# Kernel optimization log

Hardware: AMD Instinct MI355X
Metric: run time of the kernel (lower is better)

## Reference

```python
import jax, jax.numpy as jnp
import numpy as np

N, E, H, MID = 4096, 384, 6, 96  # n_refs, embed_dim, num_heads, mlp mid dim (max(E//4,32))
DH = E // H  # head dim = 64


def setup_inputs() -> dict:
    key = jax.random.key(0)
    ks = jax.random.split(key, 12)
    def w(k, shape, fan_in):
        return jax.random.normal(k, shape, jnp.float32) / np.float32(np.sqrt(fan_in))
    return {
        "low": jax.random.normal(ks[0], (N, E), jnp.float32),
        "high": jax.random.normal(ks[1], (N, E), jnp.float32),
        "ref_w": jax.random.uniform(ks[2], (N,), jnp.float32) + 0.1,
        "low_w1": w(ks[3], (E, MID), E), "low_b1": jnp.zeros((MID,), jnp.float32),
        "low_w2": w(ks[4], (MID, E), MID), "low_b2": jnp.zeros((E,), jnp.float32),
        "high_w1": w(ks[5], (E, MID), E), "high_b1": jnp.zeros((MID,), jnp.float32),
        "high_w2": w(ks[6], (MID, E), MID), "high_b2": jnp.zeros((E,), jnp.float32),
        "layer_fuse": jnp.array([0.4, 0.6], jnp.float32),
        "wqkv": w(ks[7], (E, 3 * E), E), "bqkv": jnp.zeros((3 * E,), jnp.float32),
        "wo": w(ks[8], (E, E), E), "bo": jnp.zeros((E,), jnp.float32),
        "ln_g": jnp.ones((E,), jnp.float32), "ln_b": jnp.zeros((E,), jnp.float32),
    }


def _channel_mlp(x, w1, b1, w2, b2):
    h = jax.nn.gelu(x @ w1 + b1, approximate=False)  # [N, MID]
    return x * jax.nn.sigmoid(h @ w2 + b2)           # [N, E]


def _forward(low, high, ref_w, low_w1, low_b1, low_w2, low_b2,
             high_w1, high_b1, high_w2, high_b2, layer_fuse,
             wqkv, bqkv, wo, bo, ln_g, ln_b):
    lw = jax.nn.softmax(layer_fuse)
    fused = lw[0] * _channel_mlp(low, low_w1, low_b1, low_w2, low_b2) \
          + lw[1] * _channel_mlp(high, high_w1, high_b1, high_w2, high_b2)  # [N, E]
    # single-layer MHA over the n-reference sequence (batch of 1, batch_first)
    qkv = fused @ wqkv + bqkv                      # [N, 3E]
    q, k, v = jnp.split(qkv, 3, axis=-1)
    q = q.reshape(N, H, DH).transpose(1, 0, 2)     # [H, N, DH]
    k = k.reshape(N, H, DH).transpose(1, 0, 2)
    v = v.reshape(N, H, DH).transpose(1, 0, 2)
    scores = jnp.einsum("hnd,hmd->hnm", q, k) / np.float32(np.sqrt(DH))
    attn = jax.nn.softmax(scores, axis=-1)         # [H, N, N]
    ctx = jnp.einsum("hnm,hmd->hnd", attn, v)      # [H, N, DH]
    attn_out = ctx.transpose(1, 0, 2).reshape(N, E) @ wo + bo
    x = attn_out + fused                           # residual
    mu = jnp.mean(x, axis=-1, keepdims=True)
    var = jnp.mean(jnp.square(x - mu), axis=-1, keepdims=True)
    x = (x - mu) / jnp.sqrt(var + 1e-5) * ln_g + ln_b
    w = ref_w / jnp.sum(ref_w)
    res = jnp.sum(x * w[:, None], axis=0)          # weighted mean over refs -> [E]
    return res / (jnp.linalg.norm(res) + 1e-8)


def reference(low, high, ref_w, low_w1, low_b1, low_w2, low_b2,
              high_w1, high_b1, high_w2, high_b2, layer_fuse,
              wqkv, bqkv, wo, bo, ln_g, ln_b):
    return _forward(low, high, ref_w, low_w1, low_b1, low_w2, low_b2,
                    high_w1, high_b1, high_w2, high_b2, layer_fuse,
                    wqkv, bqkv, wo, bo, ln_g, ln_b)
```

## Files before the change

kernel.cpp:

```cpp
#include <hip/hip_runtime.h>
#include <math.h>

#define Nn 4096
#define Ee 384
#define Hh 6
#define DHh 64
#define MIDm 96
#define TEe 1152
#define SPLIT 8

typedef short s16x8 __attribute__((ext_vector_type(8)));
typedef float f32x4 __attribute__((ext_vector_type(4)));
typedef float f32x16 __attribute__((ext_vector_type(16)));
typedef unsigned short ushort_t;
typedef unsigned short ushort4_t __attribute__((ext_vector_type(4)));

#define CROW(r, hf) ((((r) & 3)) + 8 * ((r) >> 2) + 4 * (hf))

__device__ __forceinline__ float gelu_exact(float x) {
    return 0.5f * x * (1.0f + erff(x * 0.70710678118654752f));
}
__device__ __forceinline__ float sigmoidf_(float x) {
    return 1.0f / (1.0f + __expf(-x));
}
__device__ __forceinline__ ushort_t f2bf(float x) {
    unsigned int u = __float_as_uint(x);
    u = (u + 0x7FFFu + ((u >> 16) & 1u)) >> 16;
    return (ushort_t)u;
}
__device__ __forceinline__ float bf2f(ushort_t u) {
    return __uint_as_float(((unsigned int)u) << 16);
}
__device__ __forceinline__ unsigned int cvtpk(float a, float b) {
    unsigned int r;
    asm("v_cvt_pk_bf16_f32 %0, %1, %2" : "=v"(r) : "v"(a), "v"(b));
    return r;
}
__device__ __forceinline__ void gld16(const ushort_t* g, ushort_t* l) {
    __builtin_amdgcn_global_load_lds(
        (const __attribute__((address_space(1))) unsigned int*)g,
        (__attribute__((address_space(3))) unsigned int*)l, 16, 0, 0);
}

#define W1L_OFF 0
#define W1H_OFF 36864
#define W2L_OFF 73728
#define W2H_OFF 110592
#define WQKV_OFF 147456
#define WO_OFF 589824

__global__ __launch_bounds__(256) void k_cvt(
    const float* __restrict__ lw1, const float* __restrict__ hw1,
    const float* __restrict__ lw2, const float* __restrict__ hw2,
    const float* __restrict__ wqkv, const float* __restrict__ wo,
    ushort_t* __restrict__ wT) {
    __shared__ float tl[32][33];
    const int b = blockIdx.x;
    const float* src;
    int R, C, doff, ti;
    if (b < 36)       { src = lw1;  R = 384; C = 96;   doff = W1L_OFF;  ti = b; }
    else if (b < 72)  { src = hw1;  R = 384; C = 96;   doff = W1H_OFF;  ti = b - 36; }
    else if (b < 108) { src = lw2;  R = 96;  C = 384;  doff = W2L_OFF;  ti = b - 72; }
    else if (b < 144) { src = hw2;  R = 96;  C = 384;  doff = W2H_OFF;  ti = b - 108; }
    else if (b < 576) { src = wqkv; R = 384; C = 1152; doff = WQKV_OFF; ti = b - 144; }
    else              { src = wo;   R = 384; C = 384;  doff = WO_OFF;   ti = b - 576; }
    const int tcn = C >> 5;
    const int tr = ti / tcn, tc = ti % tcn;
    const int col = threadIdx.x & 31, r8 = threadIdx.x >> 5;
#pragma unroll
    for (int i = 0; i < 4; i++) {
        const int row = r8 + 8 * i;
        tl[row][col] = src[(size_t)(tr * 32 + row) * C + tc * 32 + col];
    }
    __syncthreads();
#pragma unroll
    for (int i = 0; i < 4; i++) {
        const int rowp = r8 + 8 * i;
        wT[doff + (size_t)(tc * 32 + rowp) * R + tr * 32 + col] = f2bf(tl[col][rowp]);
    }
}

__global__ __launch_bounds__(256) void k_mlp(
    const float* __restrict__ low, const float* __restrict__ high,
    const float* __restrict__ lf, const ushort_t* __restrict__ wT,
    const float* __restrict__ lb1, const float* __restrict__ lb2,
    const float* __restrict__ hb1, const float* __restrict__ hb2,
    ushort_t* __restrict__ fusedb) {
    __shared__ float redsg[6144];
    __shared__ ushort_t Hs[2][16][104];
    float* red = redsg;
    ushort_t* Sg = (ushort_t*)redsg;
    const int t = threadIdx.x;
    const int w = t >> 6, l = t & 63, l15 = l & 15, g4 = l >> 4;
    const int st = w >> 1, kh = w & 1;
    const int rb = blockIdx.x * 16;
    const float* Xf = st ? high : low;
    const ushort_t* w1T = wT + (st ? W1H_OFF : W1L_OFF);
    const ushort_t* w2T = wT + (st ? W2H_OFF : W2L_OFF);
    {
        f32x4 hA[6];
#pragma unroll
        for (int nt = 0; nt < 6; nt++) hA[nt] = (f32x4){0.f, 0.f, 0.f, 0.f};
        for (int ks = 0; ks < 6; ks++) {
            const float* ap = &Xf[(size_t)(rb + l15) * 384 + kh * 192 + ks * 32 + g4 * 8];
            f32x4 a0 = *(const f32x4*)ap;
            f32x4 a1 = *(const f32x4*)(ap + 4);
            union { unsigned int uw[4]; s16x8 v; } ua;
            ua.uw[0] = cvtpk(a0[0], a0[1]);
            ua.uw[1] = cvtpk(a0[2], a0[3]);
            ua.uw[2] = cvtpk(a1[0], a1[1]);
            ua.uw[3] = cvtpk(a1[2], a1[3]);
#pragma unroll
            for (int nt = 0; nt < 6; nt++) {
                s16x8 bf = *(const s16x8*)&w1T[(nt * 16 + l15) * 384 + kh * 192 + ks * 32 + g4 * 8];
                hA[nt] = __builtin_amdgcn_mfma_f32_16x16x32_bf16(ua.v, bf, hA[nt], 0, 0, 0);
            }
        }
#pragma unroll
        for (int nt = 0; nt < 6; nt++)
#pragma unroll
            for (int r = 0; r < 4; r++)
                red[((st * 2 + kh) * 16 + g4 * 4 + r) * 96 + nt * 16 + l15] = hA[nt][r];
    }
    __syncthreads();
    for (int idx = t; idx < 2 * 16 * 96; idx += 256) {
        const int st2 = idx / 1536, rem = idx % 1536;
        const int rowm = rem / 96, mc = rem % 96;
        const float v = red[((st2 * 2) * 16 + rowm) * 96 + mc] +
                        red[((st2 * 2 + 1) * 16 + rowm) * 96 + mc] +
                        (st2 ? hb1[mc] : lb1[mc]);
        Hs[st2][rowm][mc] = f2bf(gelu_exact(v));
    }
    __syncthreads();
    {
        const float* b2p = st ? hb2 : lb2;
        f32x4 sA[12];
#pragma unroll
        for (int nt = 0; nt < 12; nt++) sA[nt] = (f32x4){0.f, 0.f, 0.f, 0.f};
#pragma unroll
        for (int ks = 0; ks < 3; ks++) {
            s16x8 af = *(const s16x8*)&Hs[st][l15][ks * 32 + g4 * 8];
#pragma unroll
            for (int nt = 0; nt < 12; nt++) {
                s16x8 bf = *(const s16x8*)&w2T[(kh * 192 + nt * 16 + l15) * 96 + ks * 32 + g4 * 8];
                sA[nt] = __builtin_amdgcn_mfma_f32_16x16x32_bf16(af, bf, sA[nt], 0, 0, 0);
            }
        }
#pragma unroll
        for (int nt = 0; nt < 12; nt++) {
            const float bb = b2p[kh * 192 + nt * 16 + l15];
#pragma unroll
            for (int r = 0; r < 4; r++)
                Sg[(st * 16 + g4 * 4 + r) * 384 + kh * 192 + nt * 16 + l15] =
                    f2bf(sigmoidf_(sA[nt][r] + bb));
        }
    }
    __syncthreads();
    {
        const float a0 = lf[0], a1 = lf[1];
        const float mx = fmaxf(a0, a1);
        const float e0 = __expf(a0 - mx), e1 = __expf(a1 - mx);
        const float inv = 1.0f / (e0 + e1);
        const float w0 = e0 * inv, w1v = e1 * inv;
        for (int base = t * 4; base < 16 * 384; base += 256 * 4) {
            const int row = base / 384, e0i = base % 384;
            const int gr = rb + row;
            f32x4 lo4 = *(const f32x4*)&low[(size_t)gr * 384 + e0i];
            f32x4 hi4 = *(const f32x4*)&high[(size_t)gr * 384 + e0i];
            ushort4_t s0 = *(const ushort4_t*)&Sg[row * 384 + e0i];
            ushort4_t s1 = *(const ushort4_t*)&Sg[(16 + row) * 384 + e0i];
            ushort4_t fb;
#pragma unroll
            for (int i = 0; i < 4; i++)
                fb[i] = f2bf(w0 * lo4[i] * bf2f(s0[i]) + w1v * hi4[i] * bf2f(s1[i]));
            *(ushort4_t*)&fusedb[(size_t)gr * 384 + e0i] = fb;
        }
    }
}

__global__ __launch_bounds__(256) void k_qkv(
    const ushort_t* __restrict__ fusedb, const ushort_t* __restrict__ wT,
    const float* __restrict__ bqkv,
    ushort_t* __restrict__ qb, ushort_t* __restrict__ kb, ushort_t* __restrict__ vtb) {
    __shared__ float tls[4][32][40];
    const int t = threadIdx.x;
    const int w = t >> 6, l = t & 63, ll = l & 31, hf = l >> 5;
    const int mh = w >> 1, nh = w & 1;
    const int rb = blockIdx.x * 64 + mh * 32;
    const int cb = blockIdx.y * 192 + nh * 96;
    const ushort_t* wq = wT + WQKV_OFF;
    f32x16 acc[3];
#pragma unroll
    for (int nt = 0; nt < 3; nt++)
#pragma unroll
        for (int r = 0; r < 16; r++) acc[nt][r] = 0.0f;
    for (int ks = 0; ks < 24; ks++) {
        s16x8 af = *(const s16x8*)&fusedb[(size_t)(rb + ll) * 384 + ks * 16 + hf * 8];
#pragma unroll
        for (int nt = 0; nt < 3; nt++) {
            s16x8 bf = *(const s16x8*)&wq[(size_t)(cb + nt * 32 + ll) * 384 + ks * 16 + hf * 8];
            acc[nt] = __builtin_amdgcn_mfma_f32_32x32x16_bf16(af, bf, acc[nt], 0, 0, 0);
        }
    }
#pragma unroll
    for (int nt = 0; nt < 3; nt++) {
        const int nb = cb + nt * 32;
        const int which = nb / 384, wn = nb % 384;
        const int hb = wn >> 6, d0 = wn & 63;
        const float bias = bqkv[nb + ll];
        if (which == 2) {
            const int d = d0 + ll;
#pragma unroll
            for (int g2 = 0; g2 < 4; g2++) {
                ushort4_t u4;
#pragma unroll
                for (int i2 = 0; i2 < 4; i2++) u4[i2] = f2bf(acc[nt][g2 * 4 + i2] + bias);
                *(ushort4_t*)&vtb[((size_t)(hb * 64 + d)) * Nn + rb + 8 * g2 + 4 * hf] = u4;
            }
        } else {
            const float sc = (which == 0) ? 0.18033688f : 1.0f;
#pragma unroll
            for (int r = 0; r < 16; r++) tls[w][CROW(r, hf)][ll] = (acc[nt][r] + bias) * sc;
            ushort_t* dst = which ? kb : qb;
            const int row2 = l >> 1, sg = l & 1;
            union { ushort_t us[16]; s16x8 v[2]; } u;
#pragma unroll
            for (int j = 0; j < 16; j++) u.us[j] = f2bf(tls[w][row2][sg * 16 + j]);
            size_t base = ((size_t)hb * Nn + rb + row2) * 64 + d0 + sg * 16;
            *(s16x8*)&dst[base] = u.v[0];
            *(s16x8*)&dst[base + 8] = u.v[1];
        }
    }
}

__global__ __launch_bounds__(512) void k_attn(
    const ushort_t* __restrict__ qb, const ushort_t* __restrict__ kb,
    const ushort_t* __restrict__ vtb, ushort_t* __restrict__ pof,
    float* __restrict__ pml) {
    __shared__ ushort_t Kt[2][4096];
    __shared__ ushort_t Vt[2][4096];
    const int t = threadIdx.x;
    const int wid8 = t >> 6, l = t & 63, ll = l & 31, hf = l >> 5;
    const int lid = blockIdx.x;
    const int xcd = lid & 7, gi = lid >> 3;
    const int pair = xcd * 6 + (gi >> 4);
    const int qt = gi & 15;
    const int h = pair % Hh, sp = pair / Hh;
    const int qrow0 = qt * 256 + wid8 * 32;
    const int srow = t >> 3;
    const int sslot = ((l & 7) ^ (l >> 3)) * 8;
    const int wch = wid8 * 512;
    const ushort_t* kbase = kb + (size_t)h * Nn * DHh;
    const ushort_t* vbase = vtb + (size_t)h * DHh * Nn;
    const int kst0 = sp * (Nn / SPLIT);
#define NT (Nn / (64 * SPLIT))
#define STAGE(B, TI) { const int ktb2 = kst0 + (TI) * 64;                                \
        gld16(kbase + (size_t)(ktb2 + srow) * DHh + sslot, &Kt[B][wch]);                 \
        gld16(vbase + (size_t)srow * Nn + ktb2 + sslot, &Vt[B][wch]); }

    s16x8 qf[4];
#pragma unroll
    for (int dc = 0; dc < 4; dc++)
        qf[dc] = *(const s16x8*)&qb[((size_t)h * Nn + qrow0 + ll) * DHh + dc * 16 + hf * 8];
    f32x16 o0, o1;
#pragma unroll
    for (int r = 0; r < 16; r++) { o0[r] = 0.0f; o1[r] = 0.0f; }
    float lsum = 0.0f;
    const int xorl = (ll & 7) << 3;

    STAGE(0, 0);
    __syncthreads();
    for (int kt = 0; kt < NT; kt++) {
        const int cur = kt & 1;
        if (kt < NT - 1) STAGE(cur ^ 1, kt + 1);
        const ushort_t* KtC = Kt[cur];
        const ushort_t* VtC = Vt[cur];
        f32x16 s0, s1;
#pragma unroll
        for (int r = 0; r < 16; r++) { s0[r] = 0.0f; s1[r] = 0.0f; }
        __builtin_amdgcn_s_setprio(1);
#pragma unroll
        for (int dc = 0; dc < 4; dc++) {
            const int colE = dc * 16 + hf * 8;
            s16x8 kf0 = *(const s16x8*)&KtC[ll * 64 + (colE ^ xorl)];
            s16x8 kf1 = *(const s16x8*)&KtC[(32 + ll) * 64 + (colE ^ xorl)];
            s0 = __builtin_amdgcn_mfma_f32_32x32x16_bf16(kf0, qf[dc], s0, 0, 0, 0);
            s1 = __builtin_amdgcn_mfma_f32_32x32x16_bf16(kf1, qf[dc], s1, 0, 0, 0);
        }
        __builtin_amdgcn_s_setprio(0);
#pragma unroll
        for (int r = 0; r < 16; r++) { s0[r] = exp2f(s0[r]); lsum += s0[r]; }
#pragma unroll
        for (int r = 0; r < 16; r++) { s1[r] = exp2f(s1[r]); lsum += s1[r]; }
#pragma unroll
        for (int ks = 0; ks < 4; ks++) {
            const f32x16 S = (ks < 2) ? s0 : s1;
            const int b = (ks & 1) * 8;
            unsigned int t1 = cvtpk(S[b + 0], S[b + 1]);
            unsigned int t3 = cvtpk(S[b + 2], S[b + 3]);
            unsigned int t2 = cvtpk(S[b + 4], S[b + 5]);
            unsigned int t4 = cvtpk(S[b + 6], S[b + 7]);
            asm("v_permlane32_swap_b32 %0, %1" : "+v"(t1), "+v"(t2));
            asm("v_permlane32_swap_b32 %0, %1" : "+v"(t3), "+v"(t4));
            union { unsigned int uw[4]; s16x8 v; } u;
            u.uw[0] = t1;
            u.uw[1] = t3;
            u.uw[2] = t2;
            u.uw[3] = t4;
            const int colE = ks * 16 + hf * 8;
            s16x8 vf0 = *(const s16x8*)&VtC[ll * 64 + (colE ^ xorl)];
            s16x8 vf1 = *(const s16x8*)&VtC[(32 + ll) * 64 + (colE ^ xorl)];
            o0 = __builtin_amdgcn_mfma_f32_32x32x16_bf16(vf0, u.v, o0, 0, 0, 0);
            o1 = __builtin_amdgcn_mfma_f32_32x32x16_bf16(vf1, u.v, o1, 0, 0, 0);
        }
        __syncthreads();
    }
    lsum += __shfl_xor(lsum, 32, 64);
#pragma unroll
    for (int r = 0; r < 16; r++) {
        const int d_a = CROW(r, hf), d_b = 32 + CROW(r, hf);
        pof[((size_t)(sp * Ee + h * 64 + d_a)) * Nn + qrow0 + ll] = f2bf(o0[r]);
        pof[((size_t)(sp * Ee + h * 64 + d_b)) * Nn + qrow0 + ll] = f2bf(o1[r]);
    }
    if (hf == 0)
        pml[((size_t)sp * Hh + h) * Nn + qrow0 + ll] = lsum;
#undef STAGE
#undef NT
}

__global__ __launch_bounds__(256) void k_oln(
    const ushort_t* __restrict__ pof, const float* __restrict__ pml,
    const ushort_t* __restrict__ wT, const float* __restrict__ bo,
    const ushort_t* __restrict__ fusedb,
    const float* __restrict__ lng, const float* __restrict__ lnb,
    const float* __restrict__ rw, float* __restrict__ part) {
    __shared__ ushort_t cx[16][384];
    __shared__ float xs[16][388];
    __shared__ float stats[16][2];
    __shared__ float dinvs[Hh][16];
    const int t = threadIdx.x;
    const int w = t >> 6, l = t & 63, l15 = l & 15, g4 = l >> 4;
    const int rb = blockIdx.x * 16;
    if (t < Hh * 16) {
        const int hh = t >> 4, qq = t & 15;
        float den = 0.0f;
#pragma unroll
        for (int s = 0; s < SPLIT; s++)
            den += pml[((size_t)s * Hh + hh) * Nn + rb + qq];
        dinvs[hh][qq] = 1.0f / den;
    }
    __syncthreads();
    for (int task = t; task < 768; task += 256) {
        const int e = task >> 1, half = task & 1;
        const int hh = e >> 6;
        float a8[8];
#pragma unroll
        for (int j = 0; j < 8; j++) a8[j] = 0.0f;
#pragma unroll
        for (int s = 0; s < SPLIT; s++) {
            s16x8 v = *(const s16x8*)&pof[((size_t)(s * Ee + e)) * Nn + rb + half * 8];
#pragma unroll
            for (int j = 0; j < 8; j++) a8[j] += bf2f((ushort_t)v[j]);
        }
#pragma unroll
        for (int j = 0; j < 8; j++) {
            const int q = half * 8 + j;
            cx[q][e ^ ((q & 7) << 3)] = f2bf(a8[j] * dinvs[hh][q]);
        }
    }
    __syncthreads();
    const ushort_t* woT = wT + WO_OFF;
    f32x4 oA[6];
#pragma unroll
    for (int nt = 0; nt < 6; nt++) oA[nt] = (f32x4){0.f, 0.f, 0.f, 0.f};
    const int xo = (l15 & 7) << 3;
    for (int ks = 0; ks < 12; ks++) {
        s16x8 af = *(const s16x8*)&cx[l15][(ks * 32 + g4 * 8) ^ xo];
#pragma unroll
        for (int nt = 0; nt < 6; nt++) {
            s16x8 bf = *(const s16x8*)&woT[(size_t)(w * 96 + nt * 16 + l15) * 384 + ks * 32 + g4 * 8];
            oA[nt] = __builtin_amdgcn_mfma_f32_16x16x32_bf16(af, bf, oA[nt], 0, 0, 0);
        }
    }
#pragma unroll
    for (int nt = 0; nt < 6; nt++) {
        const int col = w * 96 + nt * 16 + l15;
        const float bias = bo[col];
#pragma unroll
        for (int r = 0; r < 4; r++) {
            const int row = g4 * 4 + r;
            xs[row][col] = oA[nt][r] + bias + bf2f(fusedb[(size_t)(rb + row) * 384 + col]);
        }
    }
    __syncthreads();
    {
        const int row = t >> 4, j = t & 15;
        float s1 = 0.0f, s2 = 0.0f;
        for (int i = 0; i < 24; i++) {
            const float x = xs[row][j + 16 * i];
            s1 += x;
            s2 += x * x;
        }
#pragma unroll
        for (int off = 1; off < 16; off <<= 1) {
            s1 += __shfl_xor(s1, off, 64);
            s2 += __shfl_xor(s2, off, 64);
        }
        if (j == 0) {
            const float mu = s1 * (1.0f / Ee);
            const float var = s2 * (1.0f / Ee) - mu * mu;
            stats[row][0] = mu;
            stats[row][1] = rsqrtf(var + 1e-5f);
        }
    }
    __syncthreads();
    for (int c = t; c < 384; c += 256) {
        const float gt = lng[c], bb = lnb[c];
        float acc = 0.0f;
        for (int r = 0; r < 16; r++) {
            const float xn = (xs[r][c] - stats[r][0]) * stats[r][1] * gt + bb;
            acc += xn * rw[rb + r];
        }
        part[(size_t)blockIdx.x * Ee + c] = acc;
    }
}

__global__ __launch_bounds__(384) void k_final(const float* __restrict__ part,
                                               const float* __restrict__ rw,
                                               float* __restrict__ outp) {
    __shared__ float red[6], redw[6];
    const int t = threadIdx.x;
    float s = 0.0f;
    for (int b = 0; b < 256; b++) s += part[(size_t)b * Ee + t];
    float wsp = 0.0f;
    for (int i = t; i < Nn; i += 384) wsp += rw[i];
    float q2 = s * s;
#pragma unroll
    for (int off = 32; off > 0; off >>= 1) {
        q2 += __shfl_down(q2, off, 64);
        wsp += __shfl_down(wsp, off, 64);
    }
    const int wid = t >> 6, lane = t & 63;
    if (lane == 0) { red[wid] = q2; redw[wid] = wsp; }
    __syncthreads();
    float tot = 0.0f, wtot = 0.0f;
#pragma unroll
    for (int w = 0; w < 6; w++) { tot += red[w]; wtot += redw[w]; }
    outp[t] = s / (sqrtf(tot) + 1e-8f * wtot);
}

extern "C" void kernel_launch(void* const* d_in, const int* in_sizes, int n_in,
                              void* d_out, int out_size, void* d_ws, size_t ws_size,
                              hipStream_t stream) {
    const float* low  = (const float*)d_in[0];
    const float* high = (const float*)d_in[1];
    const float* rw   = (const float*)d_in[2];
    const float* lw1  = (const float*)d_in[3];
    const float* lb1  = (const float*)d_in[4];
    const float* lw2  = (const float*)d_in[5];
    const float* lb2  = (const float*)d_in[6];
    const float* hw1  = (const float*)d_in[7];
    const float* hb1  = (const float*)d_in[8];
    const float* hw2  = (const float*)d_in[9];
    const float* hb2  = (const float*)d_in[10];
    const float* lf   = (const float*)d_in[11];
    const float* wqkv = (const float*)d_in[12];
    const float* bqkv = (const float*)d_in[13];
    const float* wo   = (const float*)d_in[14];
    const float* bo   = (const float*)d_in[15];
    const float* lng  = (const float*)d_in[16];
    const float* lnb  = (const float*)d_in[17];

    float* ws = (float*)d_ws;
    const size_t NE = (size_t)Nn * Ee;
    float* pml  = ws;
    float* part = ws + 196608;
    ushort_t* u16base = (ushort_t*)(ws + 294912);
    ushort_t* fusedb = u16base;
    ushort_t* vtb    = u16base + NE;
    ushort_t* qb     = u16base + 2 * NE;
    ushort_t* kb     = u16base + 3 * NE;
    ushort_t* wT     = u16base + 4 * NE;
    ushort_t* pof    = wT + 737280;

    hipLaunchKernelGGL(k_cvt, dim3(720), dim3(256), 0, stream,
                       lw1, hw1, lw2, hw2, wqkv, wo, wT);
    hipLaunchKernelGGL(k_mlp, dim3(256), dim3(256), 0, stream,
                       low, high, lf, wT, lb1, lb2, hb1, hb2, fusedb);
    hipLaunchKernelGGL(k_qkv, dim3(64, 6), dim3(256), 0, stream,
                       fusedb, wT, bqkv, qb, kb, vtb);
    hipLaunchKernelGGL(k_attn, dim3(Hh * SPLIT * 16), dim3(512), 0, stream,
                       qb, kb, vtb, pof, pml);
    hipLaunchKernelGGL(k_oln, dim3(256), dim3(256), 0, stream,
                       pof, pml, wT, bo, fusedb, lng, lnb, rw, part);
    hipLaunchKernelGGL(k_final, dim3(1), dim3(384), 0, stream, part, rw, (float*)d_out);
}
```

Baseline: 140.1 us.

## Retile qkv/oln kernels, compute softmax denominators via MFMA, reblock partial output layout

Several changes at once. The QKV GEMM moves to smaller 128-thread blocks over 32-row tiles, doubling the grid. The output-projection/layernorm kernel moves to 512 threads with narrower per-wave column tiles. In attention, the scalar exp-sum accumulation is replaced by an extra MFMA against a ones vector, and the first score MFMA is seeded with zero instead of a zeroed register. The partial-output buffer is re-laid out into 16-query blocks so the reduction kernel reads contiguous chunks. Together these aim to improve occupancy, cut VALU work in the attention loop and make the partial reads coalesced, at the cost of one extra MFMA per step and a larger grid.

```diff
diff --git a/kernel.cpp b/kernel.cpp
--- a/kernel.cpp
+++ b/kernel.cpp
@@ -178,16 +178,15 @@
     }
 }
 
-__global__ __launch_bounds__(256) void k_qkv(
+__global__ __launch_bounds__(128) void k_qkv(
     const ushort_t* __restrict__ fusedb, const ushort_t* __restrict__ wT,
     const float* __restrict__ bqkv,
     ushort_t* __restrict__ qb, ushort_t* __restrict__ kb, ushort_t* __restrict__ vtb) {
-    __shared__ float tls[4][32][40];
+    __shared__ float tls[2][32][40];
     const int t = threadIdx.x;
     const int w = t >> 6, l = t & 63, ll = l & 31, hf = l >> 5;
-    const int mh = w >> 1, nh = w & 1;
-    const int rb = blockIdx.x * 64 + mh * 32;
-    const int cb = blockIdx.y * 192 + nh * 96;
+    const int rb = blockIdx.x * 32;
+    const int cb = blockIdx.y * 192 + w * 96;
     const ushort_t* wq = wT + WQKV_OFF;
     f32x16 acc[3];
 #pragma unroll
@@ -262,10 +261,13 @@
 #pragma unroll
     for (int dc = 0; dc < 4; dc++)
         qf[dc] = *(const s16x8*)&qb[((size_t)h * Nn + qrow0 + ll) * DHh + dc * 16 + hf * 8];
-    f32x16 o0, o1;
-#pragma unroll
-    for (int r = 0; r < 16; r++) { o0[r] = 0.0f; o1[r] = 0.0f; }
-    float lsum = 0.0f;
+    f32x16 zro;
+#pragma unroll
+    for (int r = 0; r < 16; r++) zro[r] = 0.0f;
+    s16x8 onesv;
+#pragma unroll
+    for (int i = 0; i < 8; i++) onesv[i] = (short)0x3F80;
+    f32x16 o0 = zro, o1 = zro, lacc = zro;
     const int xorl = (ll & 7) << 3;
 
     STAGE(0, 0);
@@ -275,12 +277,17 @@
         if (kt < NT - 1) STAGE(cur ^ 1, kt + 1);
         const ushort_t* KtC = Kt[cur];
         const ushort_t* VtC = Vt[cur];
+        __builtin_amdgcn_s_setprio(1);
         f32x16 s0, s1;
-#pragma unroll
-        for (int r = 0; r < 16; r++) { s0[r] = 0.0f; s1[r] = 0.0f; }
-        __builtin_amdgcn_s_setprio(1);
-#pragma unroll
-        for (int dc = 0; dc < 4; dc++) {
+        {
+            const int colE = hf * 8;
+            s16x8 kf0 = *(const s16x8*)&KtC[ll * 64 + (colE ^ xorl)];
+            s16x8 kf1 = *(const s16x8*)&KtC[(32 + ll) * 64 + (colE ^ xorl)];
+            s0 = __builtin_amdgcn_mfma_f32_32x32x16_bf16(kf0, qf[0], zro, 0, 0, 0);
+            s1 = __builtin_amdgcn_mfma_f32_32x32x16_bf16(kf1, qf[0], zro, 0, 0, 0);
+        }
+#pragma unroll
+        for (int dc = 1; dc < 4; dc++) {
             const int colE = dc * 16 + hf * 8;
             s16x8 kf0 = *(const s16x8*)&KtC[ll * 64 + (colE ^ xorl)];
             s16x8 kf1 = *(const s16x8*)&KtC[(32 + ll) * 64 + (colE ^ xorl)];
@@ -289,9 +296,9 @@
         }
         __builtin_amdgcn_s_setprio(0);
 #pragma unroll
-        for (int r = 0; r < 16; r++) { s0[r] = exp2f(s0[r]); lsum += s0[r]; }
-#pragma unroll
-        for (int r = 0; r < 16; r++) { s1[r] = exp2f(s1[r]); lsum += s1[r]; }
+        for (int r = 0; r < 16; r++) s0[r] = exp2f(s0[r]);
+#pragma unroll
+        for (int r = 0; r < 16; r++) s1[r] = exp2f(s1[r]);
 #pragma unroll
         for (int ks = 0; ks < 4; ks++) {
             const f32x16 S = (ks < 2) ? s0 : s1;
@@ -312,23 +319,25 @@
             s16x8 vf1 = *(const s16x8*)&VtC[(32 + ll) * 64 + (colE ^ xorl)];
             o0 = __builtin_amdgcn_mfma_f32_32x32x16_bf16(vf0, u.v, o0, 0, 0, 0);
             o1 = __builtin_amdgcn_mfma_f32_32x32x16_bf16(vf1, u.v, o1, 0, 0, 0);
+            lacc = __builtin_amdgcn_mfma_f32_32x32x16_bf16(onesv, u.v, lacc, 0, 0, 0);
         }
         __syncthreads();
     }
-    lsum += __shfl_xor(lsum, 32, 64);
+    const size_t bq = ((size_t)sp * 256 + (qrow0 >> 4) + (ll >> 4)) * 384;
+    const int q15 = ll & 15;
 #pragma unroll
     for (int r = 0; r < 16; r++) {
-        const int d_a = CROW(r, hf), d_b = 32 + CROW(r, hf);
-        pof[((size_t)(sp * Ee + h * 64 + d_a)) * Nn + qrow0 + ll] = f2bf(o0[r]);
-        pof[((size_t)(sp * Ee + h * 64 + d_b)) * Nn + qrow0 + ll] = f2bf(o1[r]);
+        const int e_a = h * 64 + CROW(r, hf);
+        pof[(bq + e_a) * 16 + q15] = f2bf(o0[r]);
+        pof[(bq + e_a + 32) * 16 + q15] = f2bf(o1[r]);
     }
     if (hf == 0)
-        pml[((size_t)sp * Hh + h) * Nn + qrow0 + ll] = lsum;
+        pml[((size_t)sp * Hh + h) * Nn + qrow0 + ll] = lacc[0];
 #undef STAGE
 #undef NT
 }
 
-__global__ __launch_bounds__(256) void k_oln(
+__global__ __launch_bounds__(512) void k_oln(
     const ushort_t* __restrict__ pof, const float* __restrict__ pml,
     const ushort_t* __restrict__ wT, const float* __restrict__ bo,
     const ushort_t* __restrict__ fusedb,
@@ -341,6 +350,7 @@
     const int t = threadIdx.x;
     const int w = t >> 6, l = t & 63, l15 = l & 15, g4 = l >> 4;
     const int rb = blockIdx.x * 16;
+    const int rbq = blockIdx.x;
     if (t < Hh * 16) {
         const int hh = t >> 4, qq = t & 15;
         float den = 0.0f;
@@ -350,7 +360,7 @@
         dinvs[hh][qq] = 1.0f / den;
     }
     __syncthreads();
-    for (int task = t; task < 768; task += 256) {
+    for (int task = t; task < 768; task += 512) {
         const int e = task >> 1, half = task & 1;
         const int hh = e >> 6;
         float a8[8];
@@ -358,7 +368,7 @@
         for (int j = 0; j < 8; j++) a8[j] = 0.0f;
 #pragma unroll
         for (int s = 0; s < SPLIT; s++) {
-            s16x8 v = *(const s16x8*)&pof[((size_t)(s * Ee + e)) * Nn + rb + half * 8];
+            s16x8 v = *(const s16x8*)&pof[(((size_t)s * 256 + rbq) * 384 + e) * 16 + half * 8];
 #pragma unroll
             for (int j = 0; j < 8; j++) a8[j] += bf2f((ushort_t)v[j]);
         }
@@ -370,21 +380,21 @@
     }
     __syncthreads();
     const ushort_t* woT = wT + WO_OFF;
-    f32x4 oA[6];
-#pragma unroll
-    for (int nt = 0; nt < 6; nt++) oA[nt] = (f32x4){0.f, 0.f, 0.f, 0.f};
+    f32x4 oA[3];
+#pragma unroll
+    for (int nt = 0; nt < 3; nt++) oA[nt] = (f32x4){0.f, 0.f, 0.f, 0.f};
     const int xo = (l15 & 7) << 3;
     for (int ks = 0; ks < 12; ks++) {
         s16x8 af = *(const s16x8*)&cx[l15][(ks * 32 + g4 * 8) ^ xo];
 #pragma unroll
-        for (int nt = 0; nt < 6; nt++) {
-            s16x8 bf = *(const s16x8*)&woT[(size_t)(w * 96 + nt * 16 + l15) * 384 + ks * 32 + g4 * 8];
+        for (int nt = 0; nt < 3; nt++) {
+            s16x8 bf = *(const s16x8*)&woT[(size_t)(w * 48 + nt * 16 + l15) * 384 + ks * 32 + g4 * 8];
             oA[nt] = __builtin_amdgcn_mfma_f32_16x16x32_bf16(af, bf, oA[nt], 0, 0, 0);
         }
     }
 #pragma unroll
-    for (int nt = 0; nt < 6; nt++) {
-        const int col = w * 96 + nt * 16 + l15;
+    for (int nt = 0; nt < 3; nt++) {
+        const int col = w * 48 + nt * 16 + l15;
         const float bias = bo[col];
 #pragma unroll
         for (int r = 0; r < 4; r++) {
@@ -394,15 +404,15 @@
     }
     __syncthreads();
     {
-        const int row = t >> 4, j = t & 15;
+        const int row = t >> 5, j = t & 31;
         float s1 = 0.0f, s2 = 0.0f;
-        for (int i = 0; i < 24; i++) {
-            const float x = xs[row][j + 16 * i];
+        for (int i = 0; i < 12; i++) {
+            const float x = xs[row][j + 32 * i];
             s1 += x;
             s2 += x * x;
         }
 #pragma unroll
-        for (int off = 1; off < 16; off <<= 1) {
+        for (int off = 1; off < 32; off <<= 1) {
             s1 += __shfl_xor(s1, off, 64);
             s2 += __shfl_xor(s2, off, 64);
         }
@@ -414,7 +424,7 @@
         }
     }
     __syncthreads();
-    for (int c = t; c < 384; c += 256) {
+    for (int c = t; c < 384; c += 512) {
         const float gt = lng[c], bb = lnb[c];
         float acc = 0.0f;
         for (int r = 0; r < 16; r++) {
@@ -487,11 +497,11 @@
                        lw1, hw1, lw2, hw2, wqkv, wo, wT);
     hipLaunchKernelGGL(k_mlp, dim3(256), dim3(256), 0, stream,
                        low, high, lf, wT, lb1, lb2, hb1, hb2, fusedb);
-    hipLaunchKernelGGL(k_qkv, dim3(64, 6), dim3(256), 0, stream,
+    hipLaunchKernelGGL(k_qkv, dim3(128, 6), dim3(128), 0, stream,
                        fusedb, wT, bqkv, qb, kb, vtb);
     hipLaunchKernelGGL(k_attn, dim3(Hh * SPLIT * 16), dim3(512), 0, stream,
                        qb, kb, vtb, pof, pml);
-    hipLaunchKernelGGL(k_oln, dim3(256), dim3(256), 0, stream,
+    hipLaunchKernelGGL(k_oln, dim3(256), dim3(512), 0, stream,
                        pof, pml, wT, bo, fusedb, lng, lnb, rw, part);
     hipLaunchKernelGGL(k_final, dim3(1), dim3(384), 0, stream, part, rw, (float*)d_out);
 }
```

Result: faster. 133.9 us (-4.4%).
